# Optimization experiments

Hardware: AMD Instinct MI355X
Metric: run time of the kernel (lower is better)

Reference implementation:

```python
import jax, jax.numpy as jnp
import numpy as np

D_MODEL = 768
N_HEADS = 4
D_HEAD = D_MODEL // N_HEADS
EPS = 1e-3  # keras LayerNormalization default


def gelu_tanh(x):
    return 0.5 * x * (1.0 + jnp.tanh(np.sqrt(2.0 / np.pi) * (x + 0.044715 * x ** 3)))


def layer_norm(x, g, b):
    mu = jnp.mean(x, axis=-1, keepdims=True)
    var = jnp.mean(jnp.square(x - mu), axis=-1, keepdims=True)
    return (x - mu) * jax.lax.rsqrt(var + EPS) * g + b


def setup_inputs() -> dict:
    key = jax.random.key(0)
    ks = jax.random.split(key, 12)
    B, S = 8, 1024
    x = jax.random.normal(ks[0], (B, S, D_MODEL), dtype=jnp.float32)
    # causal mask: 1 on strictly-future positions (added as mask * -1e9)
    mask = jnp.triu(jnp.ones((S, S), dtype=jnp.float32), k=1)[None, None]
    s = 0.02
    params = {
        'W1': jax.random.normal(ks[1], (D_MODEL, 3 * D_MODEL)) * s,
        'b1': jnp.zeros((3 * D_MODEL,), jnp.float32),
        'W3': jax.random.normal(ks[2], (D_MODEL, D_MODEL)) * s,
        'b3': jnp.zeros((D_MODEL,), jnp.float32),
        'W2': jax.random.normal(ks[3], (D_MODEL, 4 * D_MODEL)) * s,
        'b2': jnp.zeros((4 * D_MODEL,), jnp.float32),
        'W4': jax.random.normal(ks[4], (4 * D_MODEL, D_MODEL)) * s,
        'b4': jnp.zeros((D_MODEL,), jnp.float32),
        'g1': jnp.ones((D_MODEL,), jnp.float32),
        'be1': jnp.zeros((D_MODEL,), jnp.float32),
        'g2': jnp.ones((D_MODEL,), jnp.float32),
        'be2': jnp.zeros((D_MODEL,), jnp.float32),
    }
    return {'x': x, 'mask': mask, **params}


def reference(x, mask, W1, b1, W3, b3, W2, b2, W4, b4, g1, be1, g2, be2):
    B, S, _ = x.shape
    xn = layer_norm(x, g1, be1)
    qkv = xn @ W1 + b1                                  # [B,S,3D]
    q, k, v = jnp.split(qkv, 3, axis=-1)
    def split_heads(t):
        return t.reshape(B, S, N_HEADS, D_HEAD).transpose(0, 2, 1, 3)  # [B,H,S,dh]
    q, k, v = map(split_heads, (q, k, v))
    present = jnp.stack([k, v], axis=1)                  # [B,2,H,S,dh]
    w = jnp.einsum('bhqd,bhkd->bhqk', q, k)
    # NOTE: source divides by rsqrt(d_head) => multiplies by sqrt(d_head) (faithful bug)
    w = w * jnp.sqrt(jnp.float32(D_HEAD))
    w = w + mask * -1e9
    w = jax.nn.softmax(w, axis=-1)
    attn = jnp.einsum('bhqk,bhkd->bhqd', w, v)           # [B,H,S,dh]
    attn = attn.transpose(0, 2, 1, 3).reshape(B, S, D_MODEL)
    x = attn @ W3 + b3 + x                               # residual 1
    xn2 = layer_norm(x, g2, be2)
    h = gelu_tanh(xn2 @ W2 + b2)                         # [B,S,4D]
    x = h @ W4 + b4 + x                                  # residual 2
    return x, present
```

## Files before the change

### kernel.cpp

```cpp
#include <hip/hip_runtime.h>
#include <hip/hip_bf16.h>
#include <cstdint>

#define D_MODEL 768
#define NH 4
#define DH 192
#define SEQ 1024
#define BATCH 8

typedef __bf16 bf16x8 __attribute__((ext_vector_type(8)));
typedef float floatx4 __attribute__((ext_vector_type(4)));

__device__ __forceinline__ float bf2f(ushort u) {
    union { uint32_t i; float f; } x; x.i = ((uint32_t)u) << 16; return x.f;
}
__device__ __forceinline__ ushort f2bf(float f) {
    union { float f; uint32_t i; } x; x.f = f;
    uint32_t i = x.i;
    uint32_t r = (i + 0x7FFFu + ((i >> 16) & 1u)) >> 16;
    return (ushort)r;
}

__device__ __forceinline__ void gl_lds16(const void* g, void* l) {
    __builtin_amdgcn_global_load_lds(
        (const __attribute__((address_space(1))) uint32_t*)g,
        (__attribute__((address_space(3))) uint32_t*)l, 16, 0, 0);
}

template <int SPLIT>
__global__ void ln_kernel(const float* __restrict__ x, const float* __restrict__ g,
                          const float* __restrict__ be,
                          ushort* __restrict__ y_hi, ushort* __restrict__ y_lo) {
    int row = blockIdx.x;
    int tid = threadIdx.x;
    const float* xr = x + (size_t)row * D_MODEL;
    float v[3];
    float s = 0.f, ss = 0.f;
#pragma unroll
    for (int i = 0; i < 3; i++) {
        float t = xr[tid + i * 256];
        v[i] = t; s += t; ss += t * t;
    }
#pragma unroll
    for (int off = 32; off > 0; off >>= 1) {
        s += __shfl_down(s, off);
        ss += __shfl_down(ss, off);
    }
    __shared__ float rs[4], rss[4];
    int wid = tid >> 6;
    if ((tid & 63) == 0) { rs[wid] = s; rss[wid] = ss; }
    __syncthreads();
    s = rs[0] + rs[1] + rs[2] + rs[3];
    ss = rss[0] + rss[1] + rss[2] + rss[3];
    float mu = s * (1.f / 768.f);
    float var = ss * (1.f / 768.f) - mu * mu;
    float rstd = rsqrtf(var + 1e-3f);
#pragma unroll
    for (int i = 0; i < 3; i++) {
        int d = tid + i * 256;
        float val = (v[i] - mu) * rstd * g[d] + be[d];
        ushort hi = f2bf(val);
        y_hi[(size_t)row * D_MODEL + d] = hi;
        if (SPLIT) y_lo[(size_t)row * D_MODEL + d] = f2bf(val - bf2f(hi));
    }
}

__global__ void transpose_all_kernel(
    const float* __restrict__ W1, ushort* __restrict__ W1t_hi, ushort* __restrict__ W1t_lo,
    const float* __restrict__ W3, ushort* __restrict__ W3t,
    const float* __restrict__ W2, ushort* __restrict__ W2t,
    const float* __restrict__ W4, ushort* __restrict__ W4t) {
    __shared__ ushort th[64][65];
    __shared__ ushort tl[64][65];
    int bi = blockIdx.x;
    int tid = threadIdx.x;
    const float* W; ushort* Wt_hi; ushort* Wt_lo = nullptr; int K, N, lb;
    if (bi < 432)       { W = W1; Wt_hi = W1t_hi; Wt_lo = W1t_lo; K = 768;  N = 2304; lb = bi; }
    else if (bi < 576)  { W = W3; Wt_hi = W3t;                    K = 768;  N = 768;  lb = bi - 432; }
    else if (bi < 1152) { W = W2; Wt_hi = W2t;                    K = 768;  N = 3072; lb = bi - 576; }
    else                { W = W4; Wt_hi = W4t;                    K = 3072; N = 768;  lb = bi - 1152; }
    int nt = N >> 6;
    int bk = lb / nt, bn = lb % nt;
#pragma unroll
    for (int i = 0; i < 16; i++) {
        int lin = i * 256 + tid; int r = lin >> 6, c = lin & 63;
        float v = W[(size_t)(bk * 64 + r) * N + bn * 64 + c];
        ushort hi = f2bf(v);
        th[r][c] = hi;
        if (Wt_lo) tl[r][c] = f2bf(v - bf2f(hi));
    }
    __syncthreads();
#pragma unroll
    for (int i = 0; i < 16; i++) {
        int lin = i * 256 + tid; int r = lin >> 6, c = lin & 63;
        size_t o = (size_t)(bn * 64 + r) * K + bk * 64 + c;
        Wt_hi[o] = th[c][r];
        if (Wt_lo) Wt_lo[o] = tl[c][r];
    }
}

__global__ __launch_bounds__(256, 4) void gemm_qkv_split(
    const ushort* __restrict__ Ah, const ushort* __restrict__ Al,
    const ushort* __restrict__ Bh, const ushort* __restrict__ Bl,
    const float* __restrict__ bias,
    ushort* __restrict__ Qhg, ushort* __restrict__ Qlg, float* __restrict__ present,
    ushort* __restrict__ Khg, ushort* __restrict__ Klg, ushort* __restrict__ Vtg) {
    const int K = 768;
    __shared__ __align__(16) __bf16 sAh[128][32];
    __shared__ __align__(16) __bf16 sAl[128][32];
    __shared__ __align__(16) __bf16 sBh[128][32];
    __shared__ __align__(16) __bf16 sBl[128][32];
    int tid = threadIdx.x;
    int rowBase = blockIdx.x << 7;
    int colBase = blockIdx.y << 7;

    int wave = tid >> 6, lane = tid & 63;
    int wm = (wave & 1) << 6, wn = (wave >> 1) << 6;
    int lrow = lane & 15, q = lane >> 4;
    int lkswz = ((q ^ ((lrow >> 1) & 3)) << 3);
    floatx4 acc[4][4] = {};

    int srow = lane >> 2;
    int schunk = (lane & 3) ^ ((lane >> 3) & 3);
    const ushort* Ah0 = Ah + (size_t)(rowBase + wave * 32 + srow) * K + schunk * 8;
    const ushort* Al0 = Al + (size_t)(rowBase + wave * 32 + srow) * K + schunk * 8;
    const ushort* Bh0 = Bh + (size_t)(colBase + wave * 32 + srow) * K + schunk * 8;
    const ushort* Bl0 = Bl + (size_t)(colBase + wave * 32 + srow) * K + schunk * 8;
    const size_t r16 = (size_t)16 * K;
    int wr = wave * 32;

    const int nt = K >> 5;
    for (int t = 0; t < nt; t++) {
        if (t) __syncthreads();
        int k0 = t << 5;
        gl_lds16(Ah0 + k0, &sAh[wr][0]);  gl_lds16(Ah0 + r16 + k0, &sAh[wr + 16][0]);
        gl_lds16(Al0 + k0, &sAl[wr][0]);  gl_lds16(Al0 + r16 + k0, &sAl[wr + 16][0]);
        gl_lds16(Bh0 + k0, &sBh[wr][0]);  gl_lds16(Bh0 + r16 + k0, &sBh[wr + 16][0]);
        gl_lds16(Bl0 + k0, &sBl[wr][0]);  gl_lds16(Bl0 + r16 + k0, &sBl[wr + 16][0]);
        __syncthreads();
        bf16x8 afh[4], afl[4], bvh[4], bvl[4];
#pragma unroll
        for (int i = 0; i < 4; i++) {
            afh[i] = *(const bf16x8*)&sAh[wm + i * 16 + lrow][lkswz];
            afl[i] = *(const bf16x8*)&sAl[wm + i * 16 + lrow][lkswz];
        }
#pragma unroll
        for (int jj = 0; jj < 4; jj++) {
            bvh[jj] = *(const bf16x8*)&sBh[wn + jj * 16 + lrow][lkswz];
            bvl[jj] = *(const bf16x8*)&sBl[wn + jj * 16 + lrow][lkswz];
        }
#pragma unroll
        for (int i = 0; i < 4; i++)
#pragma unroll
            for (int jj = 0; jj < 4; jj++) {
                acc[i][jj] = __builtin_amdgcn_mfma_f32_16x16x32_bf16(afh[i], bvh[jj], acc[i][jj], 0, 0, 0);
                acc[i][jj] = __builtin_amdgcn_mfma_f32_16x16x32_bf16(afh[i], bvl[jj], acc[i][jj], 0, 0, 0);
                acc[i][jj] = __builtin_amdgcn_mfma_f32_16x16x32_bf16(afl[i], bvh[jj], acc[i][jj], 0, 0, 0);
            }
    }

    int cr = (lane >> 4) << 2;
    int cc = lane & 15;
#pragma unroll
    for (int jj = 0; jj < 4; jj++) {
        int col = colBase + wn + jj * 16 + cc;
        float bvs = bias[col];
        if (colBase < 768) {
#pragma unroll
            for (int i = 0; i < 4; i++) {
                int row0 = rowBase + wm + i * 16 + cr;
#pragma unroll
                for (int r = 0; r < 4; r++) {
                    float v = acc[i][jj][r] + bvs;
                    ushort hi = f2bf(v);
                    Qhg[(size_t)(row0 + r) * 768 + col] = hi;
                    Qlg[(size_t)(row0 + r) * 768 + col] = f2bf(v - bf2f(hi));
                }
            }
        } else if (colBase < 1536) {
            int kc = col - 768;
            int h = kc / DH, d = kc - h * DH;
#pragma unroll
            for (int i = 0; i < 4; i++) {
                int row0 = rowBase + wm + i * 16 + cr;
#pragma unroll
                for (int r = 0; r < 4; r++) {
                    int row = row0 + r;
                    int b = row >> 10, s = row & 1023;
                    float v = acc[i][jj][r] + bvs;
                    present[((size_t)((b * 2) * NH + h) * SEQ + s) * DH + d] = v;
                    float sv = v * 13.856406460551018f;
                    ushort hi = f2bf(sv);
                    Khg[(size_t)row * 768 + kc] = hi;
                    Klg[(size_t)row * 768 + kc] = f2bf(sv - bf2f(hi));
                }
            }
        } else {
            int vc = col - 1536;
            int h = vc / DH, d = vc - h * DH;
#pragma unroll
            for (int i = 0; i < 4; i++) {
                int row0 = rowBase + wm + i * 16 + cr;
#pragma unroll
                for (int r = 0; r < 4; r++) {
                    int row = row0 + r;
                    int b = row >> 10, s = row & 1023;
                    float v = acc[i][jj][r] + bvs;
                    present[((size_t)((b * 2 + 1) * NH + h) * SEQ + s) * DH + d] = v;
                    Vtg[((size_t)b * 768 + vc) * 1024 + s] = f2bf(v);
                }
            }
        }
    }
}

template <int GELU, int RES, int OUTF32, int SWAPG>
__global__ __launch_bounds__(256, 4) void gemm_bt(
    const ushort* __restrict__ A, const ushort* __restrict__ Bt,
    const float* __restrict__ bias, const float* __restrict__ resid,
    void* __restrict__ Cout, int M, int N, int K) {
    __shared__ __align__(16) __bf16 sA[2][128][32];
    __shared__ __align__(16) __bf16 sB[2][128][32];
    int tid = threadIdx.x;
    int rowBase = (SWAPG ? blockIdx.x : blockIdx.y) << 7;
    int colBase = (SWAPG ? blockIdx.y : blockIdx.x) << 7;

    int wave = tid >> 6, lane = tid & 63;
    int wm = (wave & 1) << 6, wn = (wave >> 1) << 6;
    int lrow = lane & 15, q = lane >> 4;
    int lkswz = ((q ^ ((lrow >> 1) & 3)) << 3);
    floatx4 acc[4][4] = {};

    int srow = lane >> 2;
    int schunk = (lane & 3) ^ ((lane >> 3) & 3);
    const ushort* Ag0 = A + (size_t)(rowBase + wave * 32 + srow) * K + schunk * 8;
    const ushort* Bg0 = Bt + (size_t)(colBase + wave * 32 + srow) * K + schunk * 8;
    const size_t r16 = (size_t)16 * K;
    int wr = wave * 32;

    gl_lds16(Ag0, &sA[0][wr][0]);  gl_lds16(Ag0 + r16, &sA[0][wr + 16][0]);
    gl_lds16(Bg0, &sB[0][wr][0]);  gl_lds16(Bg0 + r16, &sB[0][wr + 16][0]);
    __syncthreads();

    int nt = K >> 5;
    for (int t = 0; t < nt; t++) {
        int cur = t & 1, nb = cur ^ 1;
        if (t + 1 < nt) {
            int k0 = (t + 1) << 5;
            gl_lds16(Ag0 + k0, &sA[nb][wr][0]);  gl_lds16(Ag0 + r16 + k0, &sA[nb][wr + 16][0]);
            gl_lds16(Bg0 + k0, &sB[nb][wr][0]);  gl_lds16(Bg0 + r16 + k0, &sB[nb][wr + 16][0]);
        }
        bf16x8 af[4], bv[4];
#pragma unroll
        for (int i = 0; i < 4; i++) af[i] = *(const bf16x8*)&sA[cur][wm + i * 16 + lrow][lkswz];
#pragma unroll
        for (int jj = 0; jj < 4; jj++) bv[jj] = *(const bf16x8*)&sB[cur][wn + jj * 16 + lrow][lkswz];
#pragma unroll
        for (int i = 0; i < 4; i++)
#pragma unroll
            for (int jj = 0; jj < 4; jj++)
                acc[i][jj] = __builtin_amdgcn_mfma_f32_16x16x32_bf16(af[i], bv[jj], acc[i][jj], 0, 0, 0);
        __syncthreads();
    }
    int cr = (lane >> 4) << 2;
    int cc = lane & 15;
#pragma unroll
    for (int jj = 0; jj < 4; jj++) {
        int col = colBase + wn + jj * 16 + cc;
        float bvs = bias[col];
#pragma unroll
        for (int i = 0; i < 4; i++) {
            int row0 = rowBase + wm + i * 16 + cr;
#pragma unroll
            for (int r = 0; r < 4; r++) {
                int row = row0 + r;
                float v = acc[i][jj][r] + bvs;
                if (GELU) {
                    float u = v;
                    float z2 = -1.5957691216057308f * (u + 0.044715f * u * u * u);
                    v = u / (1.f + __expf(z2));
                }
                if (RES) v += resid[(size_t)row * N + col];
                if (OUTF32) ((float*)Cout)[(size_t)row * N + col] = v;
                else ((ushort*)Cout)[(size_t)row * N + col] = f2bf(v);
            }
        }
    }
}

__global__ __launch_bounds__(512, 2) void attn_flash(
    const ushort* __restrict__ Qhg, const ushort* __restrict__ Qlg,
    const ushort* __restrict__ Khg, const ushort* __restrict__ Klg,
    const ushort* __restrict__ Vtg, ushort* __restrict__ attn2) {
    int bi = blockIdx.x;
    int xc = bi & 7;
    int yc = bi >> 3;
    int j  = yc & 7;
    int g  = ((yc >> 3) << 3) | xc;
    int h  = g & 3;
    int b  = g >> 2;
    int tid = threadIdx.x;
    int wave = tid >> 6, lane = tid & 63;
    int l15 = lane & 15, quad = lane >> 4;
    int tile = (wave < 4) ? (15 - j) : j;
    int w16 = wave & 3;
    int s0 = tile << 6;
    int its = 2 * (15 - j) + 2;
    int myKt = (s0 + w16 * 16 + 15) >> 5;

    __shared__ __align__(16) __bf16 sKh[2][32][200];
    __shared__ __align__(16) __bf16 sKl[2][32][200];
    __shared__ __align__(16) __bf16 sVt[2][192][40];
    __shared__ __align__(16) ushort sP[8][16][40];

    const bool lo_half = (tid < 256);
    const int kr0 = tid / 24, ke0 = (tid % 24) * 8;
    const int c1 = lo_half ? (512 + tid) : (256 + tid);
    const int kr1 = c1 / 24, ke1 = (c1 % 24) * 8;
    const int vd0 = tid >> 2, ve0 = (tid & 3) * 8;
    const int vd1 = (512 + tid) >> 2, ve1 = ((512 + tid) & 3) * 8;

    const ushort* Khb = Khg + (size_t)(b * 1024) * 768 + h * 192;
    const ushort* Klb = Klg + (size_t)(b * 1024) * 768 + h * 192;
    const ushort* Vtb = Vtg + ((size_t)(b * 768) + h * 192) * 1024;
    const ushort* Bb = lo_half ? Khb : Klb;
    __bf16* pKB = lo_half ? &sKh[0][kr1][ke1] : &sKl[0][kr1][ke1];

    uint4 rA, rB, rC, rD, rE;

    rA = *(const uint4*)(Khb + (size_t)kr0 * 768 + ke0);
    rC = *(const uint4*)(Klb + (size_t)kr0 * 768 + ke0);
    rB = *(const uint4*)(Bb + (size_t)kr1 * 768 + ke1);
    rD = *(const uint4*)(Vtb + (size_t)vd0 * 1024 + ve0);
    if (lo_half) rE = *(const uint4*)(Vtb + (size_t)vd1 * 1024 + ve1);

    bf16x8 qh[6], ql[6];
    {
        int qrow = s0 + w16 * 16 + l15;
        const ushort* qph = Qhg + (size_t)(b * SEQ + qrow) * 768 + h * DH + quad * 8;
        const ushort* qpl = Qlg + (size_t)(b * SEQ + qrow) * 768 + h * DH + quad * 8;
#pragma unroll
        for (int dt = 0; dt < 6; dt++) {
            qh[dt] = *(const bf16x8*)(qph + dt * 32);
            ql[dt] = *(const bf16x8*)(qpl + dt * 32);
        }
    }

    floatx4 O[12] = {};
    float m_run[4], l_run[4];
#pragma unroll
    for (int r = 0; r < 4; r++) { m_run[r] = -1e30f; l_run[r] = 0.f; }

    *(uint4*)&sKh[0][kr0][ke0] = rA;
    *(uint4*)&sKl[0][kr0][ke0] = rC;
    *(uint4*)(pKB) = rB;
    *(uint4*)&sVt[0][vd0][ve0] = rD;
    if (lo_half) *(uint4*)&sVt[0][vd1][ve1] = rE;
    __syncthreads();

    for (int kt = 0; kt < its; kt++) {
        int cur = kt & 1;
        bool pfetch = (kt + 1 < its);
        if (pfetch) {
            int koff = (kt + 1) * 32;
            rA = *(const uint4*)(Khb + (size_t)(koff + kr0) * 768 + ke0);
            rC = *(const uint4*)(Klb + (size_t)(koff + kr0) * 768 + ke0);
            rB = *(const uint4*)(Bb + (size_t)(koff + kr1) * 768 + ke1);
            rD = *(const uint4*)(Vtb + (size_t)vd0 * 1024 + koff + ve0);
            if (lo_half) rE = *(const uint4*)(Vtb + (size_t)vd1 * 1024 + koff + ve1);
        }
        if (kt <= myKt) {
            floatx4 S0 = {}, S1 = {};
#pragma unroll
            for (int dt = 0; dt < 6; dt++) {
                bf16x8 k0h = *(const bf16x8*)&sKh[cur][l15][dt * 32 + quad * 8];
                bf16x8 k0l = *(const bf16x8*)&sKl[cur][l15][dt * 32 + quad * 8];
                bf16x8 k1h = *(const bf16x8*)&sKh[cur][16 + l15][dt * 32 + quad * 8];
                bf16x8 k1l = *(const bf16x8*)&sKl[cur][16 + l15][dt * 32 + quad * 8];
                S0 = __builtin_amdgcn_mfma_f32_16x16x32_bf16(qh[dt], k0h, S0, 0, 0, 0);
                S0 = __builtin_amdgcn_mfma_f32_16x16x32_bf16(qh[dt], k0l, S0, 0, 0, 0);
                S0 = __builtin_amdgcn_mfma_f32_16x16x32_bf16(ql[dt], k0h, S0, 0, 0, 0);
                S1 = __builtin_amdgcn_mfma_f32_16x16x32_bf16(qh[dt], k1h, S1, 0, 0, 0);
                S1 = __builtin_amdgcn_mfma_f32_16x16x32_bf16(qh[dt], k1l, S1, 0, 0, 0);
                S1 = __builtin_amdgcn_mfma_f32_16x16x32_bf16(ql[dt], k1h, S1, 0, 0, 0);
            }
            int qg = s0 + w16 * 16 + quad * 4;
            int colb = kt * 32 + l15;
            float mt[4];
#pragma unroll
            for (int r = 0; r < 4; r++) {
                float a = (colb <= qg + r) ? S0[r] : -1e30f;
                float c = (colb + 16 <= qg + r) ? S1[r] : -1e30f;
                S0[r] = a; S1[r] = c;
                mt[r] = fmaxf(a, c);
            }
#pragma unroll
            for (int m = 1; m <= 8; m <<= 1)
#pragma unroll
                for (int r = 0; r < 4; r++) mt[r] = fmaxf(mt[r], __shfl_xor(mt[r], m));
            float alpha[4], rsum[4], P0[4], P1[4];
#pragma unroll
            for (int r = 0; r < 4; r++) {
                float mn = fmaxf(m_run[r], mt[r]);
                alpha[r] = __expf(m_run[r] - mn);
                m_run[r] = mn;
                P0[r] = __expf(S0[r] - mn);
                P1[r] = __expf(S1[r] - mn);
                rsum[r] = P0[r] + P1[r];
            }
#pragma unroll
            for (int m = 1; m <= 8; m <<= 1)
#pragma unroll
                for (int r = 0; r < 4; r++) rsum[r] += __shfl_xor(rsum[r], m);
#pragma unroll
            for (int r = 0; r < 4; r++) l_run[r] = l_run[r] * alpha[r] + rsum[r];
#pragma unroll
            for (int t = 0; t < 12; t++)
#pragma unroll
                for (int r = 0; r < 4; r++) O[t][r] *= alpha[r];
#pragma unroll
            for (int r = 0; r < 4; r++) {
                sP[wave][quad * 4 + r][l15]      = f2bf(P0[r]);
                sP[wave][quad * 4 + r][16 + l15] = f2bf(P1[r]);
            }
            bf16x8 pfrag = *(const bf16x8*)&sP[wave][l15][quad * 8];
#pragma unroll
            for (int t = 0; t < 12; t++) {
                bf16x8 vf = *(const bf16x8*)&sVt[cur][t * 16 + l15][quad * 8];
                O[t] = __builtin_amdgcn_mfma_f32_16x16x32_bf16(pfrag, vf, O[t], 0, 0, 0);
            }
        }
        if (pfetch) {
            int nb = cur ^ 1;
            *(uint4*)&sKh[nb][kr0][ke0] = rA;
            *(uint4*)&sKl[nb][kr0][ke0] = rC;
            *(uint4*)(pKB + nb * 6400) = rB;
            *(uint4*)&sVt[nb][vd0][ve0] = rD;
            if (lo_half) *(uint4*)&sVt[nb][vd1][ve1] = rE;
        }
        __syncthreads();
    }

    float inv[4];
#pragma unroll
    for (int r = 0; r < 4; r++) inv[r] = 1.f / l_run[r];
    int qrow = s0 + w16 * 16 + quad * 4;
#pragma unroll
    for (int t = 0; t < 12; t++)
#pragma unroll
        for (int r = 0; r < 4; r++)
            attn2[(size_t)(b * SEQ + qrow + r) * D_MODEL + h * DH + t * 16 + l15] =
                f2bf(O[t][r] * inv[r]);
}

extern "C" void kernel_launch(void* const* d_in, const int* in_sizes, int n_in,
                              void* d_out, int out_size, void* d_ws, size_t ws_size,
                              hipStream_t stream) {
    const float* x  = (const float*)d_in[0];
    const float* W1 = (const float*)d_in[2];
    const float* b1 = (const float*)d_in[3];
    const float* W3 = (const float*)d_in[4];
    const float* b3 = (const float*)d_in[5];
    const float* W2 = (const float*)d_in[6];
    const float* b2 = (const float*)d_in[7];
    const float* W4 = (const float*)d_in[8];
    const float* b4 = (const float*)d_in[9];
    const float* g1 = (const float*)d_in[10];
    const float* be1 = (const float*)d_in[11];
    const float* g2 = (const float*)d_in[12];
    const float* be2 = (const float*)d_in[13];

    char* ws = (char*)d_ws;
    ushort* W1t_hi = (ushort*)(ws + 0);
    ushort* W1t_lo = (ushort*)(ws + 3538944);
    ushort* W3t    = (ushort*)(ws + 7077888);
    ushort* W2t    = (ushort*)(ws + 8257536);
    ushort* W4t    = (ushort*)(ws + 12976128);
    ushort* xn_hi  = (ushort*)(ws + 17694720);
    ushort* attn2  = (ushort*)(ws + 17694720);
    ushort* xn_lo  = (ushort*)(ws + 30277632);
    ushort* xn2    = (ushort*)(ws + 30277632);
    ushort* Qhg    = (ushort*)(ws + 42860544);
    ushort* Qlg    = (ushort*)(ws + 55443456);
    ushort* hbuf   = (ushort*)(ws + 42860544);
    ushort* Khg    = (ushort*)(ws + 68026368);
    ushort* Klg    = (ushort*)(ws + 80609280);
    ushort* Vtg    = (ushort*)(ws + 93192192);
    float*  x1     = (float*)(ws + 105775104);

    float* out0 = (float*)d_out;
    float* present = out0 + 6291456;

    transpose_all_kernel<<<1728, 256, 0, stream>>>(W1, W1t_hi, W1t_lo, W3, W3t, W2, W2t, W4, W4t);

    ln_kernel<1><<<8192, 256, 0, stream>>>(x, g1, be1, xn_hi, xn_lo);
    gemm_qkv_split<<<dim3(8192 / 128, 2304 / 128), 256, 0, stream>>>(
        xn_hi, xn_lo, W1t_hi, W1t_lo, b1, Qhg, Qlg, present, Khg, Klg, Vtg);
    attn_flash<<<BATCH * NH * 8, 512, 0, stream>>>(Qhg, Qlg, Khg, Klg, Vtg, attn2);
    gemm_bt<0, 1, 1, 1><<<dim3(8192 / 128, 768 / 128), 256, 0, stream>>>(
        attn2, W3t, b3, x, x1, 8192, 768, 768);
    ln_kernel<0><<<8192, 256, 0, stream>>>(x1, g2, be2, xn2, nullptr);
    gemm_bt<1, 0, 0, 1><<<dim3(8192 / 128, 3072 / 128), 256, 0, stream>>>(
        xn2, W2t, b2, nullptr, hbuf, 8192, 3072, 768);
    gemm_bt<0, 1, 1, 1><<<dim3(8192 / 128, 3072 / 128 / 4), 256, 0, stream>>>(
        hbuf, W4t, b4, x1, out0, 8192, 768, 3072);
}
```

Baseline: 481.6 us.

## Merge weight transpose with first layernorm, add nontemporal stores, setprio, raise occupancy

Folds the first layernorm into the weight-transpose launch as extra blocks, saving one kernel launch and letting the two independent jobs overlap. Writes to the present tensor and the final output use nontemporal stores so write-once data does not pollute cache. The attention MFMA sections are wrapped in s_setprio so matrix work gets issue priority. Launch bounds for the GEMMs rise from 4 to 5 waves per SIMD, which may force register spilling.

```diff
diff --git a/kernel.cpp b/kernel.cpp
--- a/kernel.cpp
+++ b/kernel.cpp
@@ -28,11 +28,11 @@
 }
 
 template <int SPLIT>
-__global__ void ln_kernel(const float* __restrict__ x, const float* __restrict__ g,
+__device__ __forceinline__ void ln_body(int row, int tid,
+                          const float* __restrict__ x, const float* __restrict__ g,
                           const float* __restrict__ be,
-                          ushort* __restrict__ y_hi, ushort* __restrict__ y_lo) {
-    int row = blockIdx.x;
-    int tid = threadIdx.x;
+                          ushort* __restrict__ y_hi, ushort* __restrict__ y_lo,
+                          float* rs, float* rss) {
     const float* xr = x + (size_t)row * D_MODEL;
     float v[3];
     float s = 0.f, ss = 0.f;
@@ -46,7 +46,6 @@
         s += __shfl_down(s, off);
         ss += __shfl_down(ss, off);
     }
-    __shared__ float rs[4], rss[4];
     int wid = tid >> 6;
     if ((tid & 63) == 0) { rs[wid] = s; rss[wid] = ss; }
     __syncthreads();
@@ -65,15 +64,30 @@
     }
 }
 
-__global__ void transpose_all_kernel(
+template <int SPLIT>
+__global__ void ln_kernel(const float* __restrict__ x, const float* __restrict__ g,
+                          const float* __restrict__ be,
+                          ushort* __restrict__ y_hi, ushort* __restrict__ y_lo) {
+    __shared__ float rs[4], rss[4];
+    ln_body<SPLIT>(blockIdx.x, threadIdx.x, x, g, be, y_hi, y_lo, rs, rss);
+}
+
+__global__ void prep_kernel(
     const float* __restrict__ W1, ushort* __restrict__ W1t_hi, ushort* __restrict__ W1t_lo,
     const float* __restrict__ W3, ushort* __restrict__ W3t,
     const float* __restrict__ W2, ushort* __restrict__ W2t,
-    const float* __restrict__ W4, ushort* __restrict__ W4t) {
+    const float* __restrict__ W4, ushort* __restrict__ W4t,
+    const float* __restrict__ x, const float* __restrict__ g1,
+    const float* __restrict__ be1, ushort* __restrict__ xn_hi, ushort* __restrict__ xn_lo) {
     __shared__ ushort th[64][65];
     __shared__ ushort tl[64][65];
+    __shared__ float rs[4], rss[4];
     int bi = blockIdx.x;
     int tid = threadIdx.x;
+    if (bi >= 1728) {
+        ln_body<1>(bi - 1728, tid, x, g1, be1, xn_hi, xn_lo, rs, rss);
+        return;
+    }
     const float* W; ushort* Wt_hi; ushort* Wt_lo = nullptr; int K, N, lb;
     if (bi < 432)       { W = W1; Wt_hi = W1t_hi; Wt_lo = W1t_lo; K = 768;  N = 2304; lb = bi; }
     else if (bi < 576)  { W = W3; Wt_hi = W3t;                    K = 768;  N = 768;  lb = bi - 432; }
@@ -99,7 +113,7 @@
     }
 }
 
-__global__ __launch_bounds__(256, 4) void gemm_qkv_split(
+__global__ __launch_bounds__(256, 5) void gemm_qkv_split(
     const ushort* __restrict__ Ah, const ushort* __restrict__ Al,
     const ushort* __restrict__ Bh, const ushort* __restrict__ Bl,
     const float* __restrict__ bias,
@@ -188,7 +202,8 @@
                     int row = row0 + r;
                     int b = row >> 10, s = row & 1023;
                     float v = acc[i][jj][r] + bvs;
-                    present[((size_t)((b * 2) * NH + h) * SEQ + s) * DH + d] = v;
+                    __builtin_nontemporal_store(v,
+                        &present[((size_t)((b * 2) * NH + h) * SEQ + s) * DH + d]);
                     float sv = v * 13.856406460551018f;
                     ushort hi = f2bf(sv);
                     Khg[(size_t)row * 768 + kc] = hi;
@@ -206,7 +221,8 @@
                     int row = row0 + r;
                     int b = row >> 10, s = row & 1023;
                     float v = acc[i][jj][r] + bvs;
-                    present[((size_t)((b * 2 + 1) * NH + h) * SEQ + s) * DH + d] = v;
+                    __builtin_nontemporal_store(v,
+                        &present[((size_t)((b * 2 + 1) * NH + h) * SEQ + s) * DH + d]);
                     Vtg[((size_t)b * 768 + vc) * 1024 + s] = f2bf(v);
                 }
             }
@@ -214,8 +230,8 @@
     }
 }
 
-template <int GELU, int RES, int OUTF32, int SWAPG>
-__global__ __launch_bounds__(256, 4) void gemm_bt(
+template <int GELU, int RES, int OUTF32, int SWAPG, int NT>
+__global__ __launch_bounds__(256, 5) void gemm_bt(
     const ushort* __restrict__ A, const ushort* __restrict__ Bt,
     const float* __restrict__ bias, const float* __restrict__ resid,
     void* __restrict__ Cout, int M, int N, int K) {
@@ -281,8 +297,13 @@
                     v = u / (1.f + __expf(z2));
                 }
                 if (RES) v += resid[(size_t)row * N + col];
-                if (OUTF32) ((float*)Cout)[(size_t)row * N + col] = v;
-                else ((ushort*)Cout)[(size_t)row * N + col] = f2bf(v);
+                if (OUTF32) {
+                    float* p = &((float*)Cout)[(size_t)row * N + col];
+                    if (NT) __builtin_nontemporal_store(v, p);
+                    else *p = v;
+                } else {
+                    ((ushort*)Cout)[(size_t)row * N + col] = f2bf(v);
+                }
             }
         }
     }
@@ -371,6 +392,7 @@
         }
         if (kt <= myKt) {
             floatx4 S0 = {}, S1 = {};
+            __builtin_amdgcn_s_setprio(1);
 #pragma unroll
             for (int dt = 0; dt < 6; dt++) {
                 bf16x8 k0h = *(const bf16x8*)&sKh[cur][l15][dt * 32 + quad * 8];
@@ -384,6 +406,7 @@
                 S1 = __builtin_amdgcn_mfma_f32_16x16x32_bf16(qh[dt], k1l, S1, 0, 0, 0);
                 S1 = __builtin_amdgcn_mfma_f32_16x16x32_bf16(ql[dt], k1h, S1, 0, 0, 0);
             }
+            __builtin_amdgcn_s_setprio(0);
             int qg = s0 + w16 * 16 + quad * 4;
             int colb = kt * 32 + l15;
             float mt[4];
@@ -424,11 +447,13 @@
                 sP[wave][quad * 4 + r][16 + l15] = f2bf(P1[r]);
             }
             bf16x8 pfrag = *(const bf16x8*)&sP[wave][l15][quad * 8];
+            __builtin_amdgcn_s_setprio(1);
 #pragma unroll
             for (int t = 0; t < 12; t++) {
                 bf16x8 vf = *(const bf16x8*)&sVt[cur][t * 16 + l15][quad * 8];
                 O[t] = __builtin_amdgcn_mfma_f32_16x16x32_bf16(pfrag, vf, O[t], 0, 0, 0);
             }
+            __builtin_amdgcn_s_setprio(0);
         }
         if (pfetch) {
             int nb = cur ^ 1;
@@ -491,17 +516,16 @@
     float* out0 = (float*)d_out;
     float* present = out0 + 6291456;
 
-    transpose_all_kernel<<<1728, 256, 0, stream>>>(W1, W1t_hi, W1t_lo, W3, W3t, W2, W2t, W4, W4t);
-
-    ln_kernel<1><<<8192, 256, 0, stream>>>(x, g1, be1, xn_hi, xn_lo);
+    prep_kernel<<<1728 + 8192, 256, 0, stream>>>(
+        W1, W1t_hi, W1t_lo, W3, W3t, W2, W2t, W4, W4t, x, g1, be1, xn_hi, xn_lo);
     gemm_qkv_split<<<dim3(8192 / 128, 2304 / 128), 256, 0, stream>>>(
         xn_hi, xn_lo, W1t_hi, W1t_lo, b1, Qhg, Qlg, present, Khg, Klg, Vtg);
     attn_flash<<<BATCH * NH * 8, 512, 0, stream>>>(Qhg, Qlg, Khg, Klg, Vtg, attn2);
-    gemm_bt<0, 1, 1, 1><<<dim3(8192 / 128, 768 / 128), 256, 0, stream>>>(
+    gemm_bt<0, 1, 1, 1, 0><<<dim3(8192 / 128, 768 / 128), 256, 0, stream>>>(
         attn2, W3t, b3, x, x1, 8192, 768, 768);
     ln_kernel<0><<<8192, 256, 0, stream>>>(x1, g2, be2, xn2, nullptr);
-    gemm_bt<1, 0, 0, 1><<<dim3(8192 / 128, 3072 / 128), 256, 0, stream>>>(
+    gemm_bt<1, 0, 0, 1, 0><<<dim3(8192 / 128, 3072 / 128), 256, 0, stream>>>(
         xn2, W2t, b2, nullptr, hbuf, 8192, 3072, 768);
-    gemm_bt<0, 1, 1, 1><<<dim3(8192 / 128, 3072 / 128 / 4), 256, 0, stream>>>(
+    gemm_bt<0, 1, 1, 1, 1><<<dim3(8192 / 128, 3072 / 128 / 4), 256, 0, stream>>>(
         hbuf, W4t, b4, x1, out0, 8192, 768, 3072);
 }
```

New measurement: 667.6 us. +38.6%, slower.
